# Performance work log

Hardware: AMD Instinct MI355X
Metric: run time of the kernel (lower is better)

## Reference

```python
import jax, jax.numpy as jnp
import numpy as np

SCORE_THRESH = 0.5
NMS_THRESH = 0.4
TOP_K = 1000  # fixed pre-NMS candidate budget (jit-safe replacement for boolean masking)
STRIDES = (8, 16, 32)
H, W = 2176, 3840


def _anchor_centers(fh, fw, stride):
    yv, xv = jnp.meshgrid(jnp.arange(fh), jnp.arange(fw), indexing='ij')
    return (jnp.stack([xv, yv], -1).reshape(-1, 2).astype(jnp.float32)) * stride  # [N,2]


def _decode_level(scores, bbox, kps, stride):
    fh, fw = H // stride, W // stride
    c = _anchor_centers(fh, fw, stride)                 # [N,2]
    s = jax.nn.sigmoid(scores.reshape(-1))              # [N]
    d = bbox.reshape(-1, 4) * stride                    # [N,4]
    boxes = jnp.concatenate([c - d[:, :2], c + d[:, 2:4]], axis=1)  # x1y1x2y2
    k = kps.reshape(-1, 5, 2) * stride + c[:, None, :]  # (x,y) pairs
    return s, boxes, k.reshape(-1, 10)


def _iou_matrix(b):
    area = (b[:, 2] - b[:, 0]) * (b[:, 3] - b[:, 1])
    lt = jnp.maximum(b[:, None, :2], b[None, :, :2])
    rb = jnp.minimum(b[:, None, 2:], b[None, :, 2:])
    wh = jnp.clip(rb - lt, 0.0)
    inter = wh[..., 0] * wh[..., 1]
    return inter / jnp.clip(area[:, None] + area[None, :] - inter, 1e-9)


def _nms_keep(iou, valid):
    n = iou.shape[0]
    ar = jnp.arange(n)

    def body(i, keep):
        sup = (iou[i] > NMS_THRESH) & (ar > i) & keep[i]
        return keep & ~sup

    return jax.lax.fori_loop(0, n, body, valid)


def reference(x, scores8, bbox8, kps8, scores16, bbox16, kps16, scores32, bbox32, kps32):
    levels = ((scores8, bbox8, kps8), (scores16, bbox16, kps16), (scores32, bbox32, kps32))
    ss, bs, ks = [], [], []
    for (s, b, k), stride in zip(levels, STRIDES):
        si, bi, ki = _decode_level(s, b, k, stride)
        ss.append(si); bs.append(bi); ks.append(ki)
    scores = jnp.concatenate(ss)   # [N_total]
    boxes = jnp.concatenate(bs)    # [N_total,4]
    kpss = jnp.concatenate(ks)     # [N_total,10]

    masked = jnp.where(scores > SCORE_THRESH, scores, -1.0)
    top_s, idx = jax.lax.top_k(masked, TOP_K)
    valid = top_s > SCORE_THRESH
    b = boxes[idx]
    k = kpss[idx]

    keep = jax.lax.stop_gradient(_nms_keep(_iou_matrix(b), valid))
    final_boxes = jnp.where(keep[:, None], b, 0.0)
    final_scores = jnp.where(keep, top_s, 0.0)
    final_kpss = jnp.where(keep[:, None], k, 0.0)
    return final_boxes, final_scores, final_kpss


def setup_inputs() -> dict:
    key = jax.random.key(0)
    ks = jax.random.split(key, 10)
    n8 = (H // 8) * (W // 8)
    n16 = (H // 16) * (W // 16)
    n32 = (H // 32) * (W // 32)
    return {
        'x': jax.random.normal(ks[0], (1, 3, H, W), jnp.float32),
        'scores8': jax.random.normal(ks[1], (1, n8, 1), jnp.float32),
        'bbox8': jax.random.uniform(ks[2], (1, n8, 4), jnp.float32),
        'kps8': jax.random.normal(ks[3], (1, n8, 10), jnp.float32),
        'scores16': jax.random.normal(ks[4], (1, n16, 1), jnp.float32),
        'bbox16': jax.random.uniform(ks[5], (1, n16, 4), jnp.float32),
        'kps16': jax.random.normal(ks[6], (1, n16, 10), jnp.float32),
        'scores32': jax.random.normal(ks[7], (1, n32, 1), jnp.float32),
        'bbox32': jax.random.uniform(ks[8], (1, n32, 4), jnp.float32),
        'kps32': jax.random.normal(ks[9], (1, n32, 10), jnp.float32),
    }
```

## Files before the change

### kernel.cpp

```cpp
#include <hip/hip_runtime.h>
#include <stdint.h>

typedef unsigned int u32;
typedef unsigned long long u64;

#define N8   130560
#define N16  32640
#define N32  8160
#define NTOT 171360
#define NTOT4 42840
#define TOPK 1000
#define NWORDS 16
#define NBINS 4096
#define BUCKET_SCALE 682.0f
#define LIST_CAP 2048
#define NBLK 168
#define NRED 32
#define RANK_BLKS 32
#define IOU_TASKS (TOPK * NWORDS)
#define IOU_BLKS 63
#define NMS_CACHE 256

#define MI_B    0
#define MI_CNT  128
#define MI_RED  256
#define MI_REDD 384
#define MI_CMP  512
#define MI_CMPD 640
#define MI_IOU  768
#define META_U32 1024

#define OFF_PART 0
#define OFF_RED  2752512
#define OFF_META 2768896
#define OFF_NZ   2772992
#define OFF_LIST 2773120
#define OFF_MASK 2789504

__device__ __forceinline__ u32 ald32(const u32* p) {
  return __hip_atomic_load(p, __ATOMIC_RELAXED, __HIP_MEMORY_SCOPE_AGENT);
}
__device__ __forceinline__ u64 ald64(const u64* p) {
  return __hip_atomic_load(p, __ATOMIC_RELAXED, __HIP_MEMORY_SCOPE_AGENT);
}
__device__ __forceinline__ void ast32(u32* p, u32 v) {
  __hip_atomic_store(p, v, __ATOMIC_RELAXED, __HIP_MEMORY_SCOPE_AGENT);
}
__device__ __forceinline__ void ast64(u64* p, u64 v) {
  __hip_atomic_store(p, v, __ATOMIC_RELAXED, __HIP_MEMORY_SCOPE_AGENT);
}

__device__ __forceinline__ u32 bucket_of(float x) {
  u32 b = (u32)(x * BUCKET_SCALE);
  return b > (NBINS - 1) ? (NBINS - 1) : b;
}

__device__ __forceinline__ float4 load_logit4(int v, const float* s8, const float* s16,
                                              const float* s32) {
  int e = v * 4;
  if (e < N8) return ((const float4*)s8)[v];
  if (e < N8 + N16) return ((const float4*)s16)[v - N8 / 4];
  return ((const float4*)s32)[v - (N8 + N16) / 4];
}

__device__ __forceinline__ bool iou_gt04(float4 a, float4 b) {
#pragma clang fp contract(off)
  float areaA = (a.z - a.x) * (a.w - a.y);
  float areaB = (b.z - b.x) * (b.w - b.y);
  float ltx = fmaxf(a.x, b.x);
  float lty = fmaxf(a.y, b.y);
  float rbx = fminf(a.z, b.z);
  float rby = fminf(a.w, b.w);
  float wx = rbx - ltx; wx = wx > 0.0f ? wx : 0.0f;
  float wy = rby - lty; wy = wy > 0.0f ? wy : 0.0f;
  float inter = wx * wy;
  float un = areaA + areaB - inter;
  un = un > 1e-9f ? un : 1e-9f;
  return (inter / un) > 0.4f;
}

__device__ __forceinline__ u64 valid_word(int w, u32 vcnt) {
  int lo = w * 64;
  if ((int)vcnt >= lo + 64) return ~0ull;
  if ((int)vcnt <= lo) return 0ull;
  return (1ull << (vcnt - (u32)lo)) - 1ull;
}

__global__ void __launch_bounds__(256) k_hist(
    const float* __restrict__ s8, const float* __restrict__ s16, const float* __restrict__ s32,
    u32* __restrict__ part, u32* __restrict__ meta, u64* __restrict__ nzWords) {
  __shared__ u32 lh[NBINS];
  int t = threadIdx.x, blk = blockIdx.x;
#pragma unroll
  for (int k = 0; k < 16; ++k) lh[k * 256 + t] = 0;
  __syncthreads();
  int v = blk * 256 + t;
  if (v < NTOT4) {
    float4 x = load_logit4(v, s8, s16, s32);
    if (x.x > 0.0f) atomicAdd(&lh[bucket_of(x.x)], 1u);
    if (x.y > 0.0f) atomicAdd(&lh[bucket_of(x.y)], 1u);
    if (x.z > 0.0f) atomicAdd(&lh[bucket_of(x.z)], 1u);
    if (x.w > 0.0f) atomicAdd(&lh[bucket_of(x.w)], 1u);
  }
  __syncthreads();
#pragma unroll
  for (int k = 0; k < 16; ++k) part[blk * NBINS + k * 256 + t] = lh[k * 256 + t];
  if (blk == 0) {
    for (int k = t; k < META_U32; k += 256) meta[k] = 0;
    if (t < NWORDS) nzWords[t] = 0ull;
  }
}

__global__ void __launch_bounds__(256) k_sel(
    const float* __restrict__ s8, const float* __restrict__ s16, const float* __restrict__ s32,
    const float* __restrict__ bb8,  const float* __restrict__ kp8,
    const float* __restrict__ bb16, const float* __restrict__ kp16,
    const float* __restrict__ bb32, const float* __restrict__ kp32,
    const u32* __restrict__ part, u32* red, u32* meta, u64* list,
    float* __restrict__ out) {
  __shared__ __align__(16) char smem[16896];
  __shared__ u32 sB, sCnt, sBase;
  __shared__ u32 cnt16[16];
  const int t = threadIdx.x, blk = blockIdx.x;
  const int v = blk * 256 + t;
  const int wave = t >> 6, lane = t & 63;

  float4 x = make_float4(-1.f, -1.f, -1.f, -1.f);
  if (v < NTOT4) x = load_logit4(v, s8, s16, s32);

  if (blk < NRED) {
    u32* lhs = (u32*)smem;
    int bin = blk * 128 + (t & 127);
    int pp = t >> 7;
    u32 acc = 0;
    for (int p = pp; p < NBLK; p += 2) acc += part[p * NBINS + bin];
    lhs[t] = acc;
    __syncthreads();
    if (t < 128) ast32(&red[blk * 128 + t], lhs[t] + lhs[t + 128]);
    __syncthreads();
    if (t == 0) {
      u32 a = __hip_atomic_fetch_add(&meta[MI_RED], 1u, __ATOMIC_RELAXED,
                                     __HIP_MEMORY_SCOPE_AGENT);
      if (a == NRED - 1) ast32(&meta[MI_REDD], 0xC0DEu);
    }
  }

  if (blk == 0) {
    if (t == 0)
      while (ald32(&meta[MI_REDD]) != 0xC0DEu) __builtin_amdgcn_s_sleep(2);
    __syncthreads();
    u32* hloc = (u32*)smem;
    u32* csum = (u32*)(smem + 16384);
#pragma unroll
    for (int k = 0; k < 16; ++k) hloc[k * 256 + t] = ald32(&red[k * 256 + t]);
    __syncthreads();
    u32 sum = 0;
    int base = t * 16;
#pragma unroll
    for (int k = 0; k < 16; ++k) sum += hloc[base + k];
    csum[t] = sum;
    __syncthreads();
    for (int off = 1; off < 256; off <<= 1) {
      u32 add = (t + off < 256) ? csum[t + off] : 0u;
      __syncthreads();
      csum[t] += add;
      __syncthreads();
    }
    u32 above = (t < 255) ? csum[t + 1] : 0u;
    if (t == 0 && csum[0] < TOPK) ast32(&meta[MI_B], 0xC0DE0000u);
    if (csum[t] >= TOPK && above < TOPK) {
      u32 cum = above, Bv = (u32)(t * 16);
      for (int b = t * 16 + 15; b >= t * 16; --b) {
        cum += hloc[b];
        if (cum >= TOPK) { Bv = (u32)b; break; }
      }
      ast32(&meta[MI_B], 0xC0DE0000u | Bv);
    }
    __syncthreads();
  }

  if (t == 0) {
    u32 pv;
    while (((pv = ald32(&meta[MI_B])) >> 16) != 0xC0DEu) __builtin_amdgcn_s_sleep(4);
    sB = pv & 0xFFFFu;
  }
  __syncthreads();
  const u32 B = sB;
  u32 win = 0;
  float c[4] = {x.x, x.y, x.z, x.w};
  if (v < NTOT4) {
#pragma unroll
    for (int j = 0; j < 4; ++j)
      if (c[j] > 0.0f && bucket_of(c[j]) >= B) win |= 1u << j;
  }
  u32 wpos[4], wcnt[4];
#pragma unroll
  for (int j = 0; j < 4; ++j) {
    u64 bal = __ballot((win >> j) & 1u);
    wcnt[j] = (u32)__popcll(bal);
    wpos[j] = (u32)__popcll(bal & ((1ull << lane) - 1ull));
  }
  if (lane == 0) {
#pragma unroll
    for (int j = 0; j < 4; ++j) cnt16[wave * 4 + j] = wcnt[j];
  }
  __syncthreads();
  if (t == 0) {
    u32 tot = 0, pre[16];
#pragma unroll
    for (int k = 0; k < 16; ++k) { pre[k] = tot; tot += cnt16[k]; }
#pragma unroll
    for (int k = 0; k < 16; ++k) cnt16[k] = pre[k];
    sBase = tot ? atomicAdd(&meta[MI_CNT], tot) : 0u;
  }
  __syncthreads();
#pragma unroll
  for (int j = 0; j < 4; ++j) {
    if ((win >> j) & 1u) {
      u32 dst = sBase + cnt16[wave * 4 + j] + wpos[j];
      if (dst < LIST_CAP) {
        u32 idx = (u32)(v * 4 + j);
        ast64(&list[dst], ((u64)__float_as_uint(c[j]) << 32) | (u64)(~idx));
      }
    }
  }
  __syncthreads();
  if (t == 0) {
    u32 a = __hip_atomic_fetch_add(&meta[MI_CMP], 1u, __ATOMIC_RELAXED,
                                   __HIP_MEMORY_SCOPE_AGENT);
    if (a == NBLK - 1) {
      u32 cc = ald32(&meta[MI_CNT]);
      if (cc > LIST_CAP) cc = LIST_CAP;
      ast32(&meta[MI_CMPD], 0xC0DE0000u | cc);
    }
  }
  if (blk >= RANK_BLKS) return;

  if (t == 0) {
    u32 pv;
    while (((pv = ald32(&meta[MI_CMPD])) >> 16) != 0xC0DEu) __builtin_amdgcn_s_sleep(4);
    sCnt = pv & 0xFFFFu;
  }
  __syncthreads();
  const u32 cnt = sCnt;
  u64* keys = (u64*)smem;
  for (int j = t; j < LIST_CAP; j += 256) keys[j] = (j < (int)cnt) ? ald64(&list[j]) : 0ull;
  __syncthreads();
  if (t >= 64) return;
  int tid = blk * 64 + t;
  if (tid < (int)cnt) {
    u64 my = keys[tid];
    int rank = 0, j = 0;
    for (; j + 4 <= (int)cnt; j += 4)
      rank += (keys[j] > my) + (keys[j + 1] > my) + (keys[j + 2] > my) + (keys[j + 3] > my);
    for (; j < (int)cnt; ++j) rank += (keys[j] > my);
    if (rank < TOPK) {
      float lx = __uint_as_float((u32)(my >> 32));
      float sc = (float)(1.0 / (1.0 + exp(-(double)lx)));
      u32 idx = ~((u32)my);
      float4 box;
      float kv[10];
      int p, xq, yq;
      float st;
      const float *bb, *kp;
      if (idx < N8) {
        st = 8.f;  p = (int)idx;              xq = p % 480; yq = p / 480; bb = bb8;  kp = kp8;
      } else if (idx < N8 + N16) {
        st = 16.f; p = (int)idx - N8;         xq = p % 240; yq = p / 240; bb = bb16; kp = kp16;
      } else {
        st = 32.f; p = (int)idx - (N8 + N16); xq = p % 120; yq = p / 120; bb = bb32; kp = kp32;
      }
      float cx = (float)xq * st, cy = (float)yq * st;
      {
#pragma clang fp contract(off)
        float d0 = bb[4 * p + 0] * st;
        float d1 = bb[4 * p + 1] * st;
        float d2 = bb[4 * p + 2] * st;
        float d3 = bb[4 * p + 3] * st;
        box.x = cx - d0; box.y = cy - d1; box.z = cx + d2; box.w = cy + d3;
        for (int q = 0; q < 10; ++q)
          kv[q] = kp[10 * p + q] * st + ((q & 1) ? cy : cx);
      }
      ((float4*)out)[rank] = box;
      out[4000 + rank] = sc;
      for (int q = 0; q < 10; ++q) out[5000 + 10 * rank + q] = kv[q];
    }
  } else if (tid < TOPK) {
    ((float4*)out)[tid] = make_float4(0.f, 0.f, 0.f, 0.f);
    out[4000 + tid] = 0.f;
    for (int q = 0; q < 10; ++q) out[5000 + 10 * tid + q] = 0.f;
  }
}

__global__ void __launch_bounds__(256) k_iou_nms(
    const u32* __restrict__ meta_ro, u32* meta, u64* nzWords, u64* mask, float* out) {
  __shared__ __align__(16) char smem[36864];
  __shared__ int isLast;
  __shared__ u32 sPc[16], sOff17[17];
  __shared__ u64 sRem[NWORDS];
  int t = threadIdx.x;
  int blk = blockIdx.x;

  float4* boxes = (float4*)smem;
  for (int r = t; r < TOPK; r += 256) boxes[r] = ((const float4*)out)[r];
  __syncthreads();
  int task = blk * 256 + t;
  if (task < IOU_TASKS) {
    int w = task / 1000;
    int i = task - w * 1000;
    float4 a = boxes[i];
    int bse = w * 64;
    int jend = (bse + 64) < TOPK ? (bse + 64) : TOPK;
    u64 bits = 0;
    for (int j = bse; j < jend; ++j)
      if (j > i && iou_gt04(a, boxes[j])) bits |= 1ull << (j - bse);
    ast64(&mask[(u64)w * 1000 + i], bits);
    if (bits) atomicOr(&nzWords[i >> 6], 1ull << (i & 63));
  }
  __syncthreads();
  if (t == 0)
    isLast = (__hip_atomic_fetch_add(&meta[MI_IOU], 1u, __ATOMIC_RELAXED,
                                     __HIP_MEMORY_SCOPE_AGENT) == (u32)(IOU_BLKS - 1));
  __syncthreads();
  if (!isLast) return;

  u32 cnt = meta_ro[MI_CMPD] & 0xFFFFu;
  const u32 vcnt = cnt < TOPK ? cnt : TOPK;
  u32* rows = (u32*)smem;
  u64* cache = (u64*)(smem + 4096);
  u64 nzv = 0;
  if (t < NWORDS) {
    nzv = ald64(&nzWords[t]) & valid_word(t, vcnt);
    sPc[t] = (u32)__popcll(nzv);
  }
  __syncthreads();
  if (t == 0) {
    u32 o = 0;
    for (int w = 0; w < NWORDS; ++w) { sOff17[w] = o; o += sPc[w]; }
    sOff17[16] = o;
  }
  __syncthreads();
  if (t < NWORDS) {
    u64 m = nzv;
    u32 o = sOff17[t];
    while (m) { int b = __builtin_ctzll(m); m &= m - 1; rows[o++] = (u32)(t * 64 + b); }
  }
  __syncthreads();
  const int S = (int)sOff17[16];
  const int Sc = S < NMS_CACHE ? S : NMS_CACHE;
  for (int idx = t; idx < Sc * NWORDS; idx += 256) {
    int s = idx >> 4, w = idx & 15;
    cache[s * NWORDS + w] = ald64(&mask[(u64)w * 1000 + rows[s]]);
  }
  __syncthreads();
  if (t < 64) {
    u64 remv = 0;
    for (int s = 0; s < S; ++s) {
      u32 row = rows[s];
      int c = (int)(row >> 6), b = (int)(row & 63);
      u64 remc = __shfl(remv, c);
      if (!((remc >> b) & 1ull)) {
        u64 m = 0;
        if (t < NWORDS)
          m = (s < NMS_CACHE) ? cache[s * NWORDS + t] : ald64(&mask[(u64)t * 1000 + row]);
        remv |= m;
      }
    }
    if (t < NWORDS) sRem[t] = valid_word(t, vcnt) & remv;
  }
  __syncthreads();
  for (int r = t; r < TOPK; r += 256) {
    if ((sRem[r >> 6] >> (r & 63)) & 1ull) {
      ((float4*)out)[r] = make_float4(0.f, 0.f, 0.f, 0.f);
      out[4000 + r] = 0.f;
      for (int q = 0; q < 10; ++q) out[5000 + 10 * r + q] = 0.f;
    }
  }
}

extern "C" void kernel_launch(void* const* d_in, const int* in_sizes, int n_in,
                              void* d_out, int out_size, void* d_ws, size_t ws_size,
                              hipStream_t stream) {
  const float* s8   = (const float*)d_in[1];
  const float* bb8  = (const float*)d_in[2];
  const float* kp8  = (const float*)d_in[3];
  const float* s16  = (const float*)d_in[4];
  const float* bb16 = (const float*)d_in[5];
  const float* kp16 = (const float*)d_in[6];
  const float* s32  = (const float*)d_in[7];
  const float* bb32 = (const float*)d_in[8];
  const float* kp32 = (const float*)d_in[9];

  char* ws = (char*)d_ws;
  u32* part    = (u32*)(ws + OFF_PART);
  u32* red     = (u32*)(ws + OFF_RED);
  u32* meta    = (u32*)(ws + OFF_META);
  u64* nzWords = (u64*)(ws + OFF_NZ);
  u64* list    = (u64*)(ws + OFF_LIST);
  u64* mask    = (u64*)(ws + OFF_MASK);
  float* out   = (float*)d_out;

  k_hist<<<NBLK, 256, 0, stream>>>(s8, s16, s32, part, meta, nzWords);
  k_sel<<<NBLK, 256, 0, stream>>>(s8, s16, s32, bb8, kp8, bb16, kp16, bb32, kp32,
                                  part, red, meta, list, out);
  k_iou_nms<<<IOU_BLKS, 256, 0, stream>>>(meta, meta, nzWords, mask, out);
}
```

Baseline: 190.8 us.

## Fuse histogram, select, decode and NMS into one persistent kernel

Merges the histogram, selection/rank-decode and IoU/NMS kernels into a single persistent kernel of 168 blocks coordinated by self-resetting global arrival counters and tagged flags. A tiny zero kernel clears the metadata first. Per-block histograms are packed as two 16-bit counts per word to halve partial-histogram traffic. The aim is to remove kernel launch gaps and the inter-kernel drain. In exchange it relies on all blocks being co-resident and adds bounded spin-waits.

```diff
diff --git a/kernel.cpp b/kernel.cpp
--- a/kernel.cpp
+++ b/kernel.cpp
@@ -20,22 +20,29 @@
 #define IOU_TASKS (TOPK * NWORDS)
 #define IOU_BLKS 63
 #define NMS_CACHE 256
-
-#define MI_B    0
-#define MI_CNT  128
-#define MI_RED  256
+#define POISON 0xAAAAAAAAu
+#define SPIN_CAP (1u << 22)
+
+
+#define MI_ARRA 0
+#define MI_REDA 128
+#define MI_ARRB 256
 #define MI_REDD 384
-#define MI_CMP  512
-#define MI_CMPD 640
-#define MI_IOU  768
-#define META_U32 1024
+#define MI_B    512
+#define MI_CNT  640
+#define MI_CMP  768
+#define MI_CMPD 896
+#define MI_DEC  1024
+#define MI_DECD 1152
+#define MI_IOU  1280
+#define META_U32 1536
 
 #define OFF_PART 0
-#define OFF_RED  2752512
-#define OFF_META 2768896
-#define OFF_NZ   2772992
-#define OFF_LIST 2773120
-#define OFF_MASK 2789504
+#define OFF_RED  1376256
+#define OFF_META 1392640
+#define OFF_NZ   1398784
+#define OFF_LIST 1398912
+#define OFF_MASK 1415296
 
 __device__ __forceinline__ u32 ald32(const u32* p) {
   return __hip_atomic_load(p, __ATOMIC_RELAXED, __HIP_MEMORY_SCOPE_AGENT);
@@ -48,6 +55,26 @@
 }
 __device__ __forceinline__ void ast64(u64* p, u64 v) {
   __hip_atomic_store(p, v, __ATOMIC_RELAXED, __HIP_MEMORY_SCOPE_AGENT);
+}
+__device__ __forceinline__ void publish(u32* p, u32 v) {
+  __hip_atomic_store(p, v, __ATOMIC_RELEASE, __HIP_MEMORY_SCOPE_AGENT);
+}
+template <int SLP>
+__device__ __forceinline__ u32 spin_tag(const u32* p) {
+  u32 v, it = 0;
+  while (((v = ald32(p)) >> 16) != 0xC0DEu) {
+    __builtin_amdgcn_s_sleep(SLP);
+    if (++it > SPIN_CAP) break;
+  }
+  return v;
+}
+__device__ __forceinline__ u32 normc(u32 v) {
+  return v >= 0x80000000u ? v - POISON : v;
+}
+__device__ __forceinline__ bool arrive_last(u32* p, u32 total) {
+  u32 old = __hip_atomic_fetch_add(p, 1u, __ATOMIC_RELAXED, __HIP_MEMORY_SCOPE_AGENT);
+  if (normc(old) == total - 1u) { ast32(p, 0u); return true; }
+  return false;
 }
 
 __device__ __forceinline__ u32 bucket_of(float x) {
@@ -86,17 +113,34 @@
   return (1ull << (vcnt - (u32)lo)) - 1ull;
 }
 
-__global__ void __launch_bounds__(256) k_hist(
+__global__ void __launch_bounds__(256) k_zero(u32* __restrict__ meta) {
+  for (int k = threadIdx.x; k < META_U32; k += 256) meta[k] = 0;
+}
+
+__global__ void __launch_bounds__(256) k_fused(
     const float* __restrict__ s8, const float* __restrict__ s16, const float* __restrict__ s32,
-    u32* __restrict__ part, u32* __restrict__ meta, u64* __restrict__ nzWords) {
-  __shared__ u32 lh[NBINS];
-  int t = threadIdx.x, blk = blockIdx.x;
+    const float* __restrict__ bb8,  const float* __restrict__ kp8,
+    const float* __restrict__ bb16, const float* __restrict__ kp16,
+    const float* __restrict__ bb32, const float* __restrict__ kp32,
+    u32* __restrict__ part, u32* red, u32* meta, u64* nzWords, u64* list, u64* mask,
+    float* out) {
+  __shared__ __align__(16) char smem[36864];
+  __shared__ u32 sB, sCntE, sCntF, sBase;
+  __shared__ u32 cnt16[16], sPc[16], sOff17[17];
+  __shared__ u64 sRem[NWORDS];
+  __shared__ int isLast;
+  const int t = threadIdx.x, blk = blockIdx.x;
+  const int wave = t >> 6, lane = t & 63;
+  const int v = blk * 256 + t;
+  u64* o64 = (u64*)out;
+
+  u32* lh = (u32*)smem;
 #pragma unroll
   for (int k = 0; k < 16; ++k) lh[k * 256 + t] = 0;
   __syncthreads();
-  int v = blk * 256 + t;
+  float4 x = make_float4(-1.f, -1.f, -1.f, -1.f);
   if (v < NTOT4) {
-    float4 x = load_logit4(v, s8, s16, s32);
+    x = load_logit4(v, s8, s16, s32);
     if (x.x > 0.0f) atomicAdd(&lh[bucket_of(x.x)], 1u);
     if (x.y > 0.0f) atomicAdd(&lh[bucket_of(x.y)], 1u);
     if (x.z > 0.0f) atomicAdd(&lh[bucket_of(x.z)], 1u);
@@ -104,55 +148,48 @@
   }
   __syncthreads();
 #pragma unroll
-  for (int k = 0; k < 16; ++k) part[blk * NBINS + k * 256 + t] = lh[k * 256 + t];
+  for (int k = 0; k < 8; ++k) {
+    int w = k * 256 + t;
+    ast32(&part[blk * 2048 + w], lh[2 * w] | (lh[2 * w + 1] << 16));
+  }
+  __syncthreads();
+  if (t == 0 && arrive_last(&meta[MI_ARRA], NBLK))
+    publish(&meta[MI_REDA], 0xC0DE0000u);
+
+  if (blk < NRED) {
+    u32* llo = (u32*)smem;
+    u32* lhi = llo + 256;
+    if (t == 0) spin_tag<2>(&meta[MI_REDA]);
+    __syncthreads();
+    int w = t & 63, pp = t >> 6;
+    u32 lo = 0, hi = 0;
+    for (int p = pp; p < NBLK; p += 4) {
+      u32 pv = ald32(&part[p * 2048 + blk * 64 + w]);
+      lo += pv & 0xFFFFu; hi += pv >> 16;
+    }
+    llo[t] = lo; lhi[t] = hi;
+    __syncthreads();
+    if (t < 64) {
+      u32 l = llo[t] + llo[64 + t] + llo[128 + t] + llo[192 + t];
+      u32 h = lhi[t] + lhi[64 + t] + lhi[128 + t] + lhi[192 + t];
+      ast32(&red[blk * 128 + 2 * t], l);
+      ast32(&red[blk * 128 + 2 * t + 1], h);
+    }
+    __syncthreads();
+    if (t == 0 && arrive_last(&meta[MI_ARRB], NRED)) {
+      ast32(&meta[MI_REDA], 0u);
+      publish(&meta[MI_REDD], 0xC0DE0000u);
+    }
+  }
+
   if (blk == 0) {
-    for (int k = t; k < META_U32; k += 256) meta[k] = 0;
-    if (t < NWORDS) nzWords[t] = 0ull;
-  }
-}
-
-__global__ void __launch_bounds__(256) k_sel(
-    const float* __restrict__ s8, const float* __restrict__ s16, const float* __restrict__ s32,
-    const float* __restrict__ bb8,  const float* __restrict__ kp8,
-    const float* __restrict__ bb16, const float* __restrict__ kp16,
-    const float* __restrict__ bb32, const float* __restrict__ kp32,
-    const u32* __restrict__ part, u32* red, u32* meta, u64* list,
-    float* __restrict__ out) {
-  __shared__ __align__(16) char smem[16896];
-  __shared__ u32 sB, sCnt, sBase;
-  __shared__ u32 cnt16[16];
-  const int t = threadIdx.x, blk = blockIdx.x;
-  const int v = blk * 256 + t;
-  const int wave = t >> 6, lane = t & 63;
-
-  float4 x = make_float4(-1.f, -1.f, -1.f, -1.f);
-  if (v < NTOT4) x = load_logit4(v, s8, s16, s32);
-
-  if (blk < NRED) {
-    u32* lhs = (u32*)smem;
-    int bin = blk * 128 + (t & 127);
-    int pp = t >> 7;
-    u32 acc = 0;
-    for (int p = pp; p < NBLK; p += 2) acc += part[p * NBINS + bin];
-    lhs[t] = acc;
-    __syncthreads();
-    if (t < 128) ast32(&red[blk * 128 + t], lhs[t] + lhs[t + 128]);
-    __syncthreads();
-    if (t == 0) {
-      u32 a = __hip_atomic_fetch_add(&meta[MI_RED], 1u, __ATOMIC_RELAXED,
-                                     __HIP_MEMORY_SCOPE_AGENT);
-      if (a == NRED - 1) ast32(&meta[MI_REDD], 0xC0DEu);
-    }
-  }
-
-  if (blk == 0) {
-    if (t == 0)
-      while (ald32(&meta[MI_REDD]) != 0xC0DEu) __builtin_amdgcn_s_sleep(2);
+    if (t == 0) { spin_tag<2>(&meta[MI_REDD]); ast32(&meta[MI_REDD], 0u); }
     __syncthreads();
     u32* hloc = (u32*)smem;
     u32* csum = (u32*)(smem + 16384);
 #pragma unroll
     for (int k = 0; k < 16; ++k) hloc[k * 256 + t] = ald32(&red[k * 256 + t]);
+    if (t < NWORDS) ast64(&nzWords[t], 0ull);
     __syncthreads();
     u32 sum = 0;
     int base = t * 16;
@@ -176,14 +213,9 @@
       }
       ast32(&meta[MI_B], 0xC0DE0000u | Bv);
     }
-    __syncthreads();
-  }
-
-  if (t == 0) {
-    u32 pv;
-    while (((pv = ald32(&meta[MI_B])) >> 16) != 0xC0DEu) __builtin_amdgcn_s_sleep(4);
-    sB = pv & 0xFFFFu;
-  }
+  }
+
+  if (t == 0) sB = spin_tag<4>(&meta[MI_B]) & 0xFFFFu;
   __syncthreads();
   const u32 B = sB;
   u32 win = 0;
@@ -211,7 +243,9 @@
     for (int k = 0; k < 16; ++k) { pre[k] = tot; tot += cnt16[k]; }
 #pragma unroll
     for (int k = 0; k < 16; ++k) cnt16[k] = pre[k];
-    sBase = tot ? atomicAdd(&meta[MI_CNT], tot) : 0u;
+    sBase = tot ? normc(__hip_atomic_fetch_add(&meta[MI_CNT], tot, __ATOMIC_RELAXED,
+                                               __HIP_MEMORY_SCOPE_AGENT))
+                : 0u;
   }
   __syncthreads();
 #pragma unroll
@@ -225,155 +259,167 @@
     }
   }
   __syncthreads();
-  if (t == 0) {
-    u32 a = __hip_atomic_fetch_add(&meta[MI_CMP], 1u, __ATOMIC_RELAXED,
-                                   __HIP_MEMORY_SCOPE_AGENT);
-    if (a == NBLK - 1) {
-      u32 cc = ald32(&meta[MI_CNT]);
-      if (cc > LIST_CAP) cc = LIST_CAP;
-      ast32(&meta[MI_CMPD], 0xC0DE0000u | cc);
-    }
-  }
-  if (blk >= RANK_BLKS) return;
-
-  if (t == 0) {
-    u32 pv;
-    while (((pv = ald32(&meta[MI_CMPD])) >> 16) != 0xC0DEu) __builtin_amdgcn_s_sleep(4);
-    sCnt = pv & 0xFFFFu;
-  }
-  __syncthreads();
-  const u32 cnt = sCnt;
-  u64* keys = (u64*)smem;
-  for (int j = t; j < LIST_CAP; j += 256) keys[j] = (j < (int)cnt) ? ald64(&list[j]) : 0ull;
-  __syncthreads();
-  if (t >= 64) return;
-  int tid = blk * 64 + t;
-  if (tid < (int)cnt) {
-    u64 my = keys[tid];
-    int rank = 0, j = 0;
-    for (; j + 4 <= (int)cnt; j += 4)
-      rank += (keys[j] > my) + (keys[j + 1] > my) + (keys[j + 2] > my) + (keys[j + 3] > my);
-    for (; j < (int)cnt; ++j) rank += (keys[j] > my);
-    if (rank < TOPK) {
-      float lx = __uint_as_float((u32)(my >> 32));
-      float sc = (float)(1.0 / (1.0 + exp(-(double)lx)));
-      u32 idx = ~((u32)my);
-      float4 box;
-      float kv[10];
-      int p, xq, yq;
-      float st;
-      const float *bb, *kp;
-      if (idx < N8) {
-        st = 8.f;  p = (int)idx;              xq = p % 480; yq = p / 480; bb = bb8;  kp = kp8;
-      } else if (idx < N8 + N16) {
-        st = 16.f; p = (int)idx - N8;         xq = p % 240; yq = p / 240; bb = bb16; kp = kp16;
-      } else {
-        st = 32.f; p = (int)idx - (N8 + N16); xq = p % 120; yq = p / 120; bb = bb32; kp = kp32;
+  if (t == 0 && arrive_last(&meta[MI_CMP], NBLK)) {
+    u32 cc = normc(ald32(&meta[MI_CNT]));
+    if (cc > LIST_CAP) cc = LIST_CAP;
+    ast32(&meta[MI_CNT], 0u);
+    ast32(&meta[MI_B], 0u);
+    publish(&meta[MI_CMPD], 0xC0DE0000u | cc);
+  }
+  if (blk >= IOU_BLKS) return;
+
+  if (blk < RANK_BLKS) {
+    if (t == 0) sCntE = spin_tag<4>(&meta[MI_CMPD]) & 0xFFFFu;
+    __syncthreads();
+    const u32 cnt = sCntE;
+    u64* keys = (u64*)smem;
+    for (int j = t; j < LIST_CAP; j += 256) keys[j] = (j < (int)cnt) ? ald64(&list[j]) : 0ull;
+    __syncthreads();
+    if (t < 64) {
+      int tid = blk * 64 + t;
+      if (tid < (int)cnt) {
+        u64 my = keys[tid];
+        int rank = 0, j = 0;
+        for (; j + 4 <= (int)cnt; j += 4)
+          rank += (keys[j] > my) + (keys[j + 1] > my) + (keys[j + 2] > my) + (keys[j + 3] > my);
+        for (; j < (int)cnt; ++j) rank += (keys[j] > my);
+        if (rank < TOPK) {
+          float lx = __uint_as_float((u32)(my >> 32));
+          float sc = (float)(1.0 / (1.0 + exp(-(double)lx)));
+          u32 idx = ~((u32)my);
+          float4 box;
+          float kv[10];
+          int p, xq, yq;
+          float st;
+          const float *bb, *kp;
+          if (idx < N8) {
+            st = 8.f;  p = (int)idx;              xq = p % 480; yq = p / 480; bb = bb8;  kp = kp8;
+          } else if (idx < N8 + N16) {
+            st = 16.f; p = (int)idx - N8;         xq = p % 240; yq = p / 240; bb = bb16; kp = kp16;
+          } else {
+            st = 32.f; p = (int)idx - (N8 + N16); xq = p % 120; yq = p / 120; bb = bb32; kp = kp32;
+          }
+          float cx = (float)xq * st, cy = (float)yq * st;
+          {
+#pragma clang fp contract(off)
+            float d0 = bb[4 * p + 0] * st;
+            float d1 = bb[4 * p + 1] * st;
+            float d2 = bb[4 * p + 2] * st;
+            float d3 = bb[4 * p + 3] * st;
+            box.x = cx - d0; box.y = cy - d1; box.z = cx + d2; box.w = cy + d3;
+            for (int q = 0; q < 10; ++q)
+              kv[q] = kp[10 * p + q] * st + ((q & 1) ? cy : cx);
+          }
+          ast64(&o64[2 * rank],     ((u64)__float_as_uint(box.y) << 32) | __float_as_uint(box.x));
+          ast64(&o64[2 * rank + 1], ((u64)__float_as_uint(box.w) << 32) | __float_as_uint(box.z));
+          ast32(&((u32*)out)[4000 + rank], __float_as_uint(sc));
+          int wb = 2500 + 5 * rank;
+#pragma unroll
+          for (int q = 0; q < 5; ++q)
+            ast64(&o64[wb + q],
+                  ((u64)__float_as_uint(kv[2 * q + 1]) << 32) | __float_as_uint(kv[2 * q]));
+        }
+      } else if (tid < TOPK) {
+        ast64(&o64[2 * tid], 0ull); ast64(&o64[2 * tid + 1], 0ull);
+        ast32(&((u32*)out)[4000 + tid], 0u);
+        int wb = 2500 + 5 * tid;
+#pragma unroll
+        for (int q = 0; q < 5; ++q) ast64(&o64[wb + q], 0ull);
       }
-      float cx = (float)xq * st, cy = (float)yq * st;
-      {
-#pragma clang fp contract(off)
-        float d0 = bb[4 * p + 0] * st;
-        float d1 = bb[4 * p + 1] * st;
-        float d2 = bb[4 * p + 2] * st;
-        float d3 = bb[4 * p + 3] * st;
-        box.x = cx - d0; box.y = cy - d1; box.z = cx + d2; box.w = cy + d3;
-        for (int q = 0; q < 10; ++q)
-          kv[q] = kp[10 * p + q] * st + ((q & 1) ? cy : cx);
+    }
+    __syncthreads();
+    if (t == 0 && arrive_last(&meta[MI_DEC], RANK_BLKS)) {
+      ast32(&meta[MI_CMPD], 0u);
+      publish(&meta[MI_DECD], 0xC0DE0000u | cnt);
+    }
+  }
+
+  if (t == 0) sCntF = spin_tag<4>(&meta[MI_DECD]) & 0xFFFFu;
+  __syncthreads();
+  {
+    float4* boxes = (float4*)smem;
+    for (int r = t; r < TOPK; r += 256) {
+      u64 a = ald64(&o64[2 * r]), b = ald64(&o64[2 * r + 1]);
+      float4 bx;
+      bx.x = __uint_as_float((u32)a); bx.y = __uint_as_float((u32)(a >> 32));
+      bx.z = __uint_as_float((u32)b); bx.w = __uint_as_float((u32)(b >> 32));
+      boxes[r] = bx;
+    }
+    __syncthreads();
+    int task = blk * 256 + t;
+    if (task < IOU_TASKS) {
+      int w = task / 1000;
+      int i = task - w * 1000;
+      float4 a = boxes[i];
+      int bse = w * 64;
+      int jend = (bse + 64) < TOPK ? (bse + 64) : TOPK;
+      u64 bits = 0;
+      for (int j = bse; j < jend; ++j)
+        if (j > i && iou_gt04(a, boxes[j])) bits |= 1ull << (j - bse);
+      ast64(&mask[(u64)w * 1000 + i], bits);
+      if (bits) atomicOr(&nzWords[i >> 6], 1ull << (i & 63));
+    }
+    __syncthreads();
+    if (t == 0) {
+      bool lastF = arrive_last(&meta[MI_IOU], IOU_BLKS);
+      if (lastF) ast32(&meta[MI_DECD], 0u);
+      isLast = lastF ? 1 : 0;
+    }
+    __syncthreads();
+    if (!isLast) return;
+
+    const u32 vcnt = sCntF < TOPK ? sCntF : TOPK;
+    u32* rows = (u32*)smem;
+    u64* cache = (u64*)(smem + 4096);
+    u64 nzv = 0;
+    if (t < NWORDS) {
+      nzv = ald64(&nzWords[t]) & valid_word(t, vcnt);
+      sPc[t] = (u32)__popcll(nzv);
+    }
+    __syncthreads();
+    if (t == 0) {
+      u32 o = 0;
+      for (int w = 0; w < NWORDS; ++w) { sOff17[w] = o; o += sPc[w]; }
+      sOff17[16] = o;
+    }
+    __syncthreads();
+    if (t < NWORDS) {
+      u64 m = nzv;
+      u32 o = sOff17[t];
+      while (m) { int b = __builtin_ctzll(m); m &= m - 1; rows[o++] = (u32)(t * 64 + b); }
+    }
+    __syncthreads();
+    const int S = (int)sOff17[16];
+    const int Sc = S < NMS_CACHE ? S : NMS_CACHE;
+    for (int idx = t; idx < Sc * NWORDS; idx += 256) {
+      int s = idx >> 4, w = idx & 15;
+      cache[s * NWORDS + w] = ald64(&mask[(u64)w * 1000 + rows[s]]);
+    }
+    __syncthreads();
+    if (t < 64) {
+      u64 remv = 0;
+      for (int s = 0; s < S; ++s) {
+        u32 row = rows[s];
+        int cc = (int)(row >> 6), b = (int)(row & 63);
+        u64 remc = __shfl(remv, cc);
+        if (!((remc >> b) & 1ull)) {
+          u64 m = 0;
+          if (t < NWORDS)
+            m = (s < NMS_CACHE) ? cache[s * NWORDS + t] : ald64(&mask[(u64)t * 1000 + row]);
+          remv |= m;
+        }
       }
-      ((float4*)out)[rank] = box;
-      out[4000 + rank] = sc;
-      for (int q = 0; q < 10; ++q) out[5000 + 10 * rank + q] = kv[q];
-    }
-  } else if (tid < TOPK) {
-    ((float4*)out)[tid] = make_float4(0.f, 0.f, 0.f, 0.f);
-    out[4000 + tid] = 0.f;
-    for (int q = 0; q < 10; ++q) out[5000 + 10 * tid + q] = 0.f;
-  }
-}
-
-__global__ void __launch_bounds__(256) k_iou_nms(
-    const u32* __restrict__ meta_ro, u32* meta, u64* nzWords, u64* mask, float* out) {
-  __shared__ __align__(16) char smem[36864];
-  __shared__ int isLast;
-  __shared__ u32 sPc[16], sOff17[17];
-  __shared__ u64 sRem[NWORDS];
-  int t = threadIdx.x;
-  int blk = blockIdx.x;
-
-  float4* boxes = (float4*)smem;
-  for (int r = t; r < TOPK; r += 256) boxes[r] = ((const float4*)out)[r];
-  __syncthreads();
-  int task = blk * 256 + t;
-  if (task < IOU_TASKS) {
-    int w = task / 1000;
-    int i = task - w * 1000;
-    float4 a = boxes[i];
-    int bse = w * 64;
-    int jend = (bse + 64) < TOPK ? (bse + 64) : TOPK;
-    u64 bits = 0;
-    for (int j = bse; j < jend; ++j)
-      if (j > i && iou_gt04(a, boxes[j])) bits |= 1ull << (j - bse);
-    ast64(&mask[(u64)w * 1000 + i], bits);
-    if (bits) atomicOr(&nzWords[i >> 6], 1ull << (i & 63));
-  }
-  __syncthreads();
-  if (t == 0)
-    isLast = (__hip_atomic_fetch_add(&meta[MI_IOU], 1u, __ATOMIC_RELAXED,
-                                     __HIP_MEMORY_SCOPE_AGENT) == (u32)(IOU_BLKS - 1));
-  __syncthreads();
-  if (!isLast) return;
-
-  u32 cnt = meta_ro[MI_CMPD] & 0xFFFFu;
-  const u32 vcnt = cnt < TOPK ? cnt : TOPK;
-  u32* rows = (u32*)smem;
-  u64* cache = (u64*)(smem + 4096);
-  u64 nzv = 0;
-  if (t < NWORDS) {
-    nzv = ald64(&nzWords[t]) & valid_word(t, vcnt);
-    sPc[t] = (u32)__popcll(nzv);
-  }
-  __syncthreads();
-  if (t == 0) {
-    u32 o = 0;
-    for (int w = 0; w < NWORDS; ++w) { sOff17[w] = o; o += sPc[w]; }
-    sOff17[16] = o;
-  }
-  __syncthreads();
-  if (t < NWORDS) {
-    u64 m = nzv;
-    u32 o = sOff17[t];
-    while (m) { int b = __builtin_ctzll(m); m &= m - 1; rows[o++] = (u32)(t * 64 + b); }
-  }
-  __syncthreads();
-  const int S = (int)sOff17[16];
-  const int Sc = S < NMS_CACHE ? S : NMS_CACHE;
-  for (int idx = t; idx < Sc * NWORDS; idx += 256) {
-    int s = idx >> 4, w = idx & 15;
-    cache[s * NWORDS + w] = ald64(&mask[(u64)w * 1000 + rows[s]]);
-  }
-  __syncthreads();
-  if (t < 64) {
-    u64 remv = 0;
-    for (int s = 0; s < S; ++s) {
-      u32 row = rows[s];
-      int c = (int)(row >> 6), b = (int)(row & 63);
-      u64 remc = __shfl(remv, c);
-      if (!((remc >> b) & 1ull)) {
-        u64 m = 0;
-        if (t < NWORDS)
-          m = (s < NMS_CACHE) ? cache[s * NWORDS + t] : ald64(&mask[(u64)t * 1000 + row]);
-        remv |= m;
+      if (t < NWORDS) sRem[t] = valid_word(t, vcnt) & remv;
+    }
+    __syncthreads();
+    for (int r = t; r < TOPK; r += 256) {
+      if ((sRem[r >> 6] >> (r & 63)) & 1ull) {
+        ast64(&o64[2 * r], 0ull); ast64(&o64[2 * r + 1], 0ull);
+        ast32(&((u32*)out)[4000 + r], 0u);
+        int wb = 2500 + 5 * r;
+#pragma unroll
+        for (int q = 0; q < 5; ++q) ast64(&o64[wb + q], 0ull);
       }
-    }
-    if (t < NWORDS) sRem[t] = valid_word(t, vcnt) & remv;
-  }
-  __syncthreads();
-  for (int r = t; r < TOPK; r += 256) {
-    if ((sRem[r >> 6] >> (r & 63)) & 1ull) {
-      ((float4*)out)[r] = make_float4(0.f, 0.f, 0.f, 0.f);
-      out[4000 + r] = 0.f;
-      for (int q = 0; q < 10; ++q) out[5000 + 10 * r + q] = 0.f;
     }
   }
 }
@@ -400,8 +446,7 @@
   u64* mask    = (u64*)(ws + OFF_MASK);
   float* out   = (float*)d_out;
 
-  k_hist<<<NBLK, 256, 0, stream>>>(s8, s16, s32, part, meta, nzWords);
-  k_sel<<<NBLK, 256, 0, stream>>>(s8, s16, s32, bb8, kp8, bb16, kp16, bb32, kp32,
-                                  part, red, meta, list, out);
-  k_iou_nms<<<IOU_BLKS, 256, 0, stream>>>(meta, meta, nzWords, mask, out);
-}
+  k_zero<<<1, 256, 0, stream>>>(meta);
+  k_fused<<<NBLK, 256, 0, stream>>>(s8, s16, s32, bb8, kp8, bb16, kp16, bb32, kp32,
+                                    part, red, meta, nzWords, list, mask, out);
+}
```

Measured after the change: 198.8 us. 1.04x slower.

## Split fused spin-wait pipeline into seven kernels with parallel rank and packed histogram

Applied to the files above, without the earlier changes.

Replaces the grid-wide spin-wait handshakes (atomic counters plus sleep loops) in the fused selection and IOU/NMS kernels with separate kernel launches: histogram, reduce, threshold find, compaction, rank, IOU mask, and single-block NMS. The per-block partial histograms are packed as two 16-bit counts per word, halving partial-histogram traffic. The rank stage now splits each candidate's comparison loop across 8 thread slices over 63 blocks instead of 64 threads per block over 32 blocks. The change trades spin-wait latency and serialized last-block work for the fixed cost of extra launches. The 16-bit packing assumes per-block bin counts stay under 65536.

```diff
diff --git a/kernel.cpp b/kernel.cpp
--- a/kernel.cpp
+++ b/kernel.cpp
@@ -13,42 +13,26 @@
 #define NWORDS 16
 #define NBINS 4096
 #define BUCKET_SCALE 682.0f
-#define LIST_CAP 2048
-#define NBLK 168
-#define NRED 32
-#define RANK_BLKS 32
+#define LIST_CAP 2016
+#define CPB 32
+#define HIST_BLKS 168
+#define RED_BLKS 32
+#define RANK_BLKS 63
+#define IOU_BLKS 63
 #define IOU_TASKS (TOPK * NWORDS)
-#define IOU_BLKS 63
 #define NMS_CACHE 256
 
-#define MI_B    0
-#define MI_CNT  128
-#define MI_RED  256
-#define MI_REDD 384
-#define MI_CMP  512
-#define MI_CMPD 640
-#define MI_IOU  768
-#define META_U32 1024
+
+#define MI_B   0
+#define MI_CNT 1
+#define META_U32 256
 
 #define OFF_PART 0
-#define OFF_RED  2752512
-#define OFF_META 2768896
-#define OFF_NZ   2772992
-#define OFF_LIST 2773120
-#define OFF_MASK 2789504
-
-__device__ __forceinline__ u32 ald32(const u32* p) {
-  return __hip_atomic_load(p, __ATOMIC_RELAXED, __HIP_MEMORY_SCOPE_AGENT);
-}
-__device__ __forceinline__ u64 ald64(const u64* p) {
-  return __hip_atomic_load(p, __ATOMIC_RELAXED, __HIP_MEMORY_SCOPE_AGENT);
-}
-__device__ __forceinline__ void ast32(u32* p, u32 v) {
-  __hip_atomic_store(p, v, __ATOMIC_RELAXED, __HIP_MEMORY_SCOPE_AGENT);
-}
-__device__ __forceinline__ void ast64(u64* p, u64 v) {
-  __hip_atomic_store(p, v, __ATOMIC_RELAXED, __HIP_MEMORY_SCOPE_AGENT);
-}
+#define OFF_RED  1376256
+#define OFF_META 1392640
+#define OFF_NZ   1393664
+#define OFF_LIST 1393792
+#define OFF_MASK 1409920
 
 __device__ __forceinline__ u32 bucket_of(float x) {
   u32 b = (u32)(x * BUCKET_SCALE);
@@ -86,11 +70,11 @@
   return (1ull << (vcnt - (u32)lo)) - 1ull;
 }
 
-__global__ void __launch_bounds__(256) k_hist(
+__global__ void __launch_bounds__(256) k1_hist(
     const float* __restrict__ s8, const float* __restrict__ s16, const float* __restrict__ s32,
-    u32* __restrict__ part, u32* __restrict__ meta, u64* __restrict__ nzWords) {
+    u32* __restrict__ part, u32* __restrict__ meta, u64* __restrict__ nz) {
   __shared__ u32 lh[NBINS];
-  int t = threadIdx.x, blk = blockIdx.x;
+  const int t = threadIdx.x, blk = blockIdx.x;
 #pragma unroll
   for (int k = 0; k < 16; ++k) lh[k * 256 + t] = 0;
   __syncthreads();
@@ -104,95 +88,86 @@
   }
   __syncthreads();
 #pragma unroll
-  for (int k = 0; k < 16; ++k) part[blk * NBINS + k * 256 + t] = lh[k * 256 + t];
+  for (int k = 0; k < 8; ++k) {
+    int w = k * 256 + t;
+    part[blk * 2048 + w] = lh[2 * w] | (lh[2 * w + 1] << 16);
+  }
   if (blk == 0) {
-    for (int k = t; k < META_U32; k += 256) meta[k] = 0;
-    if (t < NWORDS) nzWords[t] = 0ull;
-  }
-}
-
-__global__ void __launch_bounds__(256) k_sel(
+    if (t < META_U32) meta[t] = 0;
+    if (t < NWORDS) nz[t] = 0ull;
+  }
+}
+
+__global__ void __launch_bounds__(256) k2_reduce(
+    const u32* __restrict__ part, u32* __restrict__ red) {
+  __shared__ u32 llo[256], lhi[256];
+  const int t = threadIdx.x, blk = blockIdx.x;
+  const int w = t & 63, pp = t >> 6;
+  u32 lo = 0, hi = 0;
+  for (int p = pp; p < HIST_BLKS; p += 4) {
+    u32 pv = part[p * 2048 + blk * 64 + w];
+    lo += pv & 0xFFFFu; hi += pv >> 16;
+  }
+  llo[t] = lo; lhi[t] = hi;
+  __syncthreads();
+  if (t < 64) {
+    u32 l = llo[t] + llo[64 + t] + llo[128 + t] + llo[192 + t];
+    u32 h = lhi[t] + lhi[64 + t] + lhi[128 + t] + lhi[192 + t];
+    red[blk * 128 + 2 * t] = l;
+    red[blk * 128 + 2 * t + 1] = h;
+  }
+}
+
+__global__ void __launch_bounds__(256) k3_findb(
+    const u32* __restrict__ red, u32* __restrict__ meta) {
+  __shared__ u32 hloc[NBINS];
+  __shared__ u32 csum[256];
+  const int t = threadIdx.x;
+#pragma unroll
+  for (int k = 0; k < 16; ++k) hloc[k * 256 + t] = red[k * 256 + t];
+  __syncthreads();
+  u32 sum = 0;
+  int base = t * 16;
+#pragma unroll
+  for (int k = 0; k < 16; ++k) sum += hloc[base + k];
+  csum[t] = sum;
+  __syncthreads();
+  for (int off = 1; off < 256; off <<= 1) {
+    u32 add = (t + off < 256) ? csum[t + off] : 0u;
+    __syncthreads();
+    csum[t] += add;
+    __syncthreads();
+  }
+  u32 above = (t < 255) ? csum[t + 1] : 0u;
+  if (t == 0 && csum[0] < TOPK) meta[MI_B] = 0u;
+  if (csum[t] >= TOPK && above < TOPK) {
+    u32 cum = above, Bv = (u32)(t * 16);
+    for (int b = t * 16 + 15; b >= t * 16; --b) {
+      cum += hloc[b];
+      if (cum >= TOPK) { Bv = (u32)b; break; }
+    }
+    meta[MI_B] = Bv;
+  }
+}
+
+__global__ void __launch_bounds__(256) k4_compact(
     const float* __restrict__ s8, const float* __restrict__ s16, const float* __restrict__ s32,
-    const float* __restrict__ bb8,  const float* __restrict__ kp8,
-    const float* __restrict__ bb16, const float* __restrict__ kp16,
-    const float* __restrict__ bb32, const float* __restrict__ kp32,
-    const u32* __restrict__ part, u32* red, u32* meta, u64* list,
-    float* __restrict__ out) {
-  __shared__ __align__(16) char smem[16896];
-  __shared__ u32 sB, sCnt, sBase;
+    u32* __restrict__ meta, u64* __restrict__ list) {
+  __shared__ u32 sB, sBase;
   __shared__ u32 cnt16[16];
   const int t = threadIdx.x, blk = blockIdx.x;
+  const int wave = t >> 6, lane = t & 63;
   const int v = blk * 256 + t;
-  const int wave = t >> 6, lane = t & 63;
-
+  if (t == 0) sB = meta[MI_B];
   float4 x = make_float4(-1.f, -1.f, -1.f, -1.f);
   if (v < NTOT4) x = load_logit4(v, s8, s16, s32);
-
-  if (blk < NRED) {
-    u32* lhs = (u32*)smem;
-    int bin = blk * 128 + (t & 127);
-    int pp = t >> 7;
-    u32 acc = 0;
-    for (int p = pp; p < NBLK; p += 2) acc += part[p * NBINS + bin];
-    lhs[t] = acc;
-    __syncthreads();
-    if (t < 128) ast32(&red[blk * 128 + t], lhs[t] + lhs[t + 128]);
-    __syncthreads();
-    if (t == 0) {
-      u32 a = __hip_atomic_fetch_add(&meta[MI_RED], 1u, __ATOMIC_RELAXED,
-                                     __HIP_MEMORY_SCOPE_AGENT);
-      if (a == NRED - 1) ast32(&meta[MI_REDD], 0xC0DEu);
-    }
-  }
-
-  if (blk == 0) {
-    if (t == 0)
-      while (ald32(&meta[MI_REDD]) != 0xC0DEu) __builtin_amdgcn_s_sleep(2);
-    __syncthreads();
-    u32* hloc = (u32*)smem;
-    u32* csum = (u32*)(smem + 16384);
-#pragma unroll
-    for (int k = 0; k < 16; ++k) hloc[k * 256 + t] = ald32(&red[k * 256 + t]);
-    __syncthreads();
-    u32 sum = 0;
-    int base = t * 16;
-#pragma unroll
-    for (int k = 0; k < 16; ++k) sum += hloc[base + k];
-    csum[t] = sum;
-    __syncthreads();
-    for (int off = 1; off < 256; off <<= 1) {
-      u32 add = (t + off < 256) ? csum[t + off] : 0u;
-      __syncthreads();
-      csum[t] += add;
-      __syncthreads();
-    }
-    u32 above = (t < 255) ? csum[t + 1] : 0u;
-    if (t == 0 && csum[0] < TOPK) ast32(&meta[MI_B], 0xC0DE0000u);
-    if (csum[t] >= TOPK && above < TOPK) {
-      u32 cum = above, Bv = (u32)(t * 16);
-      for (int b = t * 16 + 15; b >= t * 16; --b) {
-        cum += hloc[b];
-        if (cum >= TOPK) { Bv = (u32)b; break; }
-      }
-      ast32(&meta[MI_B], 0xC0DE0000u | Bv);
-    }
-    __syncthreads();
-  }
-
-  if (t == 0) {
-    u32 pv;
-    while (((pv = ald32(&meta[MI_B])) >> 16) != 0xC0DEu) __builtin_amdgcn_s_sleep(4);
-    sB = pv & 0xFFFFu;
-  }
   __syncthreads();
   const u32 B = sB;
+  float c[4] = {x.x, x.y, x.z, x.w};
   u32 win = 0;
-  float c[4] = {x.x, x.y, x.z, x.w};
-  if (v < NTOT4) {
-#pragma unroll
-    for (int j = 0; j < 4; ++j)
-      if (c[j] > 0.0f && bucket_of(c[j]) >= B) win |= 1u << j;
-  }
+#pragma unroll
+  for (int j = 0; j < 4; ++j)
+    if (c[j] > 0.0f && bucket_of(c[j]) >= B) win |= 1u << j;
   u32 wpos[4], wcnt[4];
 #pragma unroll
   for (int j = 0; j < 4; ++j) {
@@ -220,88 +195,93 @@
       u32 dst = sBase + cnt16[wave * 4 + j] + wpos[j];
       if (dst < LIST_CAP) {
         u32 idx = (u32)(v * 4 + j);
-        ast64(&list[dst], ((u64)__float_as_uint(c[j]) << 32) | (u64)(~idx));
+        list[dst] = ((u64)__float_as_uint(c[j]) << 32) | (u64)(~idx);
       }
     }
   }
-  __syncthreads();
-  if (t == 0) {
-    u32 a = __hip_atomic_fetch_add(&meta[MI_CMP], 1u, __ATOMIC_RELAXED,
-                                   __HIP_MEMORY_SCOPE_AGENT);
-    if (a == NBLK - 1) {
-      u32 cc = ald32(&meta[MI_CNT]);
-      if (cc > LIST_CAP) cc = LIST_CAP;
-      ast32(&meta[MI_CMPD], 0xC0DE0000u | cc);
-    }
-  }
-  if (blk >= RANK_BLKS) return;
-
-  if (t == 0) {
-    u32 pv;
-    while (((pv = ald32(&meta[MI_CMPD])) >> 16) != 0xC0DEu) __builtin_amdgcn_s_sleep(4);
-    sCnt = pv & 0xFFFFu;
-  }
+}
+
+__global__ void __launch_bounds__(256) k5_rank(
+    const u32* __restrict__ meta, const u64* __restrict__ list,
+    const float* __restrict__ bb8,  const float* __restrict__ kp8,
+    const float* __restrict__ bb16, const float* __restrict__ kp16,
+    const float* __restrict__ bb32, const float* __restrict__ kp32,
+    float* __restrict__ out) {
+  __shared__ __align__(16) u64 keys[LIST_CAP];
+  __shared__ u32 rpart[256];
+  __shared__ u32 sCnt;
+  const int t = threadIdx.x, blk = blockIdx.x;
+  if (t == 0) { u32 cc = meta[MI_CNT]; sCnt = cc > LIST_CAP ? LIST_CAP : cc; }
   __syncthreads();
   const u32 cnt = sCnt;
-  u64* keys = (u64*)smem;
-  for (int j = t; j < LIST_CAP; j += 256) keys[j] = (j < (int)cnt) ? ald64(&list[j]) : 0ull;
-  __syncthreads();
-  if (t >= 64) return;
-  int tid = blk * 64 + t;
-  if (tid < (int)cnt) {
-    u64 my = keys[tid];
-    int rank = 0, j = 0;
-    for (; j + 4 <= (int)cnt; j += 4)
-      rank += (keys[j] > my) + (keys[j + 1] > my) + (keys[j + 2] > my) + (keys[j + 3] > my);
-    for (; j < (int)cnt; ++j) rank += (keys[j] > my);
-    if (rank < TOPK) {
-      float lx = __uint_as_float((u32)(my >> 32));
-      float sc = (float)(1.0 / (1.0 + exp(-(double)lx)));
-      u32 idx = ~((u32)my);
-      float4 box;
-      float kv[10];
-      int p, xq, yq;
-      float st;
-      const float *bb, *kp;
-      if (idx < N8) {
-        st = 8.f;  p = (int)idx;              xq = p % 480; yq = p / 480; bb = bb8;  kp = kp8;
-      } else if (idx < N8 + N16) {
-        st = 16.f; p = (int)idx - N8;         xq = p % 240; yq = p / 240; bb = bb16; kp = kp16;
-      } else {
-        st = 32.f; p = (int)idx - (N8 + N16); xq = p % 120; yq = p / 120; bb = bb32; kp = kp32;
+  for (int j = t; j < LIST_CAP; j += 256) keys[j] = (j < (int)cnt) ? list[j] : 0ull;
+  __syncthreads();
+  {
+    const int ci = t & 31, sl = t >> 5;
+    const int c = blk * CPB + ci;
+    const int chunk = ((int)cnt + 7) >> 3;
+    int lo = sl * chunk; if (lo > (int)cnt) lo = (int)cnt;
+    int hi = lo + chunk; if (hi > (int)cnt) hi = (int)cnt;
+    u64 my = keys[c];
+    int r = 0, j = lo;
+    for (; j + 4 <= hi; j += 4)
+      r += (keys[j] > my) + (keys[j + 1] > my) + (keys[j + 2] > my) + (keys[j + 3] > my);
+    for (; j < hi; ++j) r += (keys[j] > my);
+    rpart[t] = (u32)r;
+  }
+  __syncthreads();
+  if (t < CPB) {
+    const int c = blk * CPB + t;
+    if (c < (int)cnt) {
+      int rank = 0;
+#pragma unroll
+      for (int q = 0; q < 8; ++q) rank += (int)rpart[t + 32 * q];
+      if (rank < TOPK) {
+        u64 my = keys[c];
+        float lx = __uint_as_float((u32)(my >> 32));
+        float sc = (float)(1.0 / (1.0 + exp(-(double)lx)));
+        u32 idx = ~((u32)my);
+        float4 box;
+        float kv[10];
+        int p, xq, yq;
+        float st;
+        const float *bb, *kp;
+        if (idx < N8) {
+          st = 8.f;  p = (int)idx;              xq = p % 480; yq = p / 480; bb = bb8;  kp = kp8;
+        } else if (idx < N8 + N16) {
+          st = 16.f; p = (int)idx - N8;         xq = p % 240; yq = p / 240; bb = bb16; kp = kp16;
+        } else {
+          st = 32.f; p = (int)idx - (N8 + N16); xq = p % 120; yq = p / 120; bb = bb32; kp = kp32;
+        }
+        float cx = (float)xq * st, cy = (float)yq * st;
+        {
+#pragma clang fp contract(off)
+          float d0 = bb[4 * p + 0] * st;
+          float d1 = bb[4 * p + 1] * st;
+          float d2 = bb[4 * p + 2] * st;
+          float d3 = bb[4 * p + 3] * st;
+          box.x = cx - d0; box.y = cy - d1; box.z = cx + d2; box.w = cy + d3;
+          for (int q = 0; q < 10; ++q)
+            kv[q] = kp[10 * p + q] * st + ((q & 1) ? cy : cx);
+        }
+        ((float4*)out)[rank] = box;
+        out[4000 + rank] = sc;
+#pragma unroll
+        for (int q = 0; q < 10; ++q) out[5000 + 10 * rank + q] = kv[q];
       }
-      float cx = (float)xq * st, cy = (float)yq * st;
-      {
-#pragma clang fp contract(off)
-        float d0 = bb[4 * p + 0] * st;
-        float d1 = bb[4 * p + 1] * st;
-        float d2 = bb[4 * p + 2] * st;
-        float d3 = bb[4 * p + 3] * st;
-        box.x = cx - d0; box.y = cy - d1; box.z = cx + d2; box.w = cy + d3;
-        for (int q = 0; q < 10; ++q)
-          kv[q] = kp[10 * p + q] * st + ((q & 1) ? cy : cx);
-      }
-      ((float4*)out)[rank] = box;
-      out[4000 + rank] = sc;
-      for (int q = 0; q < 10; ++q) out[5000 + 10 * rank + q] = kv[q];
-    }
-  } else if (tid < TOPK) {
-    ((float4*)out)[tid] = make_float4(0.f, 0.f, 0.f, 0.f);
-    out[4000 + tid] = 0.f;
-    for (int q = 0; q < 10; ++q) out[5000 + 10 * tid + q] = 0.f;
-  }
-}
-
-__global__ void __launch_bounds__(256) k_iou_nms(
-    const u32* __restrict__ meta_ro, u32* meta, u64* nzWords, u64* mask, float* out) {
-  __shared__ __align__(16) char smem[36864];
-  __shared__ int isLast;
-  __shared__ u32 sPc[16], sOff17[17];
-  __shared__ u64 sRem[NWORDS];
-  int t = threadIdx.x;
-  int blk = blockIdx.x;
-
-  float4* boxes = (float4*)smem;
+    } else if (c < TOPK) {
+      ((float4*)out)[c] = make_float4(0.f, 0.f, 0.f, 0.f);
+      out[4000 + c] = 0.f;
+#pragma unroll
+      for (int q = 0; q < 10; ++q) out[5000 + 10 * c + q] = 0.f;
+    }
+  }
+}
+
+__global__ void __launch_bounds__(256) k6_iou(
+    const float* __restrict__ out, u64* __restrict__ mask, u64* __restrict__ nz) {
+  __shared__ __align__(16) float4 boxes[TOPK];
+  const int t = threadIdx.x, blk = blockIdx.x;
   for (int r = t; r < TOPK; r += 256) boxes[r] = ((const float4*)out)[r];
   __syncthreads();
   int task = blk * 256 + t;
@@ -314,23 +294,26 @@
     u64 bits = 0;
     for (int j = bse; j < jend; ++j)
       if (j > i && iou_gt04(a, boxes[j])) bits |= 1ull << (j - bse);
-    ast64(&mask[(u64)w * 1000 + i], bits);
-    if (bits) atomicOr(&nzWords[i >> 6], 1ull << (i & 63));
-  }
-  __syncthreads();
-  if (t == 0)
-    isLast = (__hip_atomic_fetch_add(&meta[MI_IOU], 1u, __ATOMIC_RELAXED,
-                                     __HIP_MEMORY_SCOPE_AGENT) == (u32)(IOU_BLKS - 1));
-  __syncthreads();
-  if (!isLast) return;
-
-  u32 cnt = meta_ro[MI_CMPD] & 0xFFFFu;
-  const u32 vcnt = cnt < TOPK ? cnt : TOPK;
+    mask[(u64)w * 1000 + i] = bits;
+    if (bits) atomicOr(&nz[i >> 6], 1ull << (i & 63));
+  }
+}
+
+__global__ void __launch_bounds__(256) k7_nms(
+    const u32* __restrict__ meta, const u64* __restrict__ nzWords,
+    const u64* __restrict__ mask, float* __restrict__ out) {
+  __shared__ __align__(16) char smem[36864];
+  __shared__ u32 sPc[16], sOff17[17];
+  __shared__ u64 sRem[NWORDS];
+  const int t = threadIdx.x;
+  u32 cc = meta[MI_CNT];
+  if (cc > LIST_CAP) cc = LIST_CAP;
+  const u32 vcnt = cc < TOPK ? cc : TOPK;
   u32* rows = (u32*)smem;
   u64* cache = (u64*)(smem + 4096);
   u64 nzv = 0;
   if (t < NWORDS) {
-    nzv = ald64(&nzWords[t]) & valid_word(t, vcnt);
+    nzv = nzWords[t] & valid_word(t, vcnt);
     sPc[t] = (u32)__popcll(nzv);
   }
   __syncthreads();
@@ -350,7 +333,7 @@
   const int Sc = S < NMS_CACHE ? S : NMS_CACHE;
   for (int idx = t; idx < Sc * NWORDS; idx += 256) {
     int s = idx >> 4, w = idx & 15;
-    cache[s * NWORDS + w] = ald64(&mask[(u64)w * 1000 + rows[s]]);
+    cache[s * NWORDS + w] = mask[(u64)w * 1000 + rows[s]];
   }
   __syncthreads();
   if (t < 64) {
@@ -362,7 +345,7 @@
       if (!((remc >> b) & 1ull)) {
         u64 m = 0;
         if (t < NWORDS)
-          m = (s < NMS_CACHE) ? cache[s * NWORDS + t] : ald64(&mask[(u64)t * 1000 + row]);
+          m = (s < NMS_CACHE) ? cache[s * NWORDS + t] : mask[(u64)t * 1000 + row];
         remv |= m;
       }
     }
@@ -373,6 +356,7 @@
     if ((sRem[r >> 6] >> (r & 63)) & 1ull) {
       ((float4*)out)[r] = make_float4(0.f, 0.f, 0.f, 0.f);
       out[4000 + r] = 0.f;
+#pragma unroll
       for (int q = 0; q < 10; ++q) out[5000 + 10 * r + q] = 0.f;
     }
   }
@@ -400,8 +384,11 @@
   u64* mask    = (u64*)(ws + OFF_MASK);
   float* out   = (float*)d_out;
 
-  k_hist<<<NBLK, 256, 0, stream>>>(s8, s16, s32, part, meta, nzWords);
-  k_sel<<<NBLK, 256, 0, stream>>>(s8, s16, s32, bb8, kp8, bb16, kp16, bb32, kp32,
-                                  part, red, meta, list, out);
-  k_iou_nms<<<IOU_BLKS, 256, 0, stream>>>(meta, meta, nzWords, mask, out);
-}
+  k1_hist<<<HIST_BLKS, 256, 0, stream>>>(s8, s16, s32, part, meta, nzWords);
+  k2_reduce<<<RED_BLKS, 256, 0, stream>>>(part, red);
+  k3_findb<<<1, 256, 0, stream>>>(red, meta);
+  k4_compact<<<HIST_BLKS, 256, 0, stream>>>(s8, s16, s32, meta, list);
+  k5_rank<<<RANK_BLKS, 256, 0, stream>>>(meta, list, bb8, kp8, bb16, kp16, bb32, kp32, out);
+  k6_iou<<<IOU_BLKS, 256, 0, stream>>>(out, mask, nzWords);
+  k7_nms<<<1, 256, 0, stream>>>(meta, nzWords, mask, out);
+}
```

New measurement: 178.0 us. -6.7%, faster.
